# Kernel optimization log

Measured on AMD Instinct MI355X. Metric: run time of the kernel, lower is better.

Reference implementation:

```python
import jax, jax.numpy as jnp
import numpy as np

B, N, H = 128, 256, 1024


def setup_inputs() -> dict:
    key = jax.random.key(0)
    ks = jax.random.split(key, 10)
    s = 1.0 / np.sqrt(H)
    return {
        "encoder_outputs": jax.random.normal(ks[0], (B, N, H), jnp.float32),
        "W_ih": jax.random.normal(ks[1], (4 * H, H), jnp.float32) * s,
        "W_hh": jax.random.normal(ks[2], (4 * H, H), jnp.float32) * s,
        "b_ih": jax.random.normal(ks[3], (4 * H,), jnp.float32) * s,
        "b_hh": jax.random.normal(ks[4], (4 * H,), jnp.float32) * s,
        "Wa": jax.random.normal(ks[5], (H, H), jnp.float32) * s,
        "Ua": jax.random.normal(ks[6], (H, H), jnp.float32) * s,
        "v": jax.random.normal(ks[7], (H,), jnp.float32) * s,
        "start_token": jax.random.uniform(ks[8], (H,), jnp.float32, -0.1, 0.1),
        "end_token": jax.random.uniform(ks[9], (H,), jnp.float32, -0.1, 0.1),
    }


def reference(encoder_outputs, W_ih, W_hh, b_ih, b_hh, Wa, Ua, v, start_token, end_token):
    b, n, h = encoder_outputs.shape
    # extended encoder outputs: [B, N+1, H] (end token appended)
    ext = jnp.concatenate([encoder_outputs, jnp.broadcast_to(end_token, (b, 1, h))], axis=1)
    enc_Wa = ext @ Wa.T  # loop-invariant W_a projection, [B, N+1, H]

    def step(carry, _):
        hx, cx, mask, x = carry
        # LSTMCell
        gates = x @ W_ih.T + b_ih + hx @ W_hh.T + b_hh  # [B, 4H]
        i_g, f_g, g_g, o_g = jnp.split(gates, 4, axis=1)
        cx = jax.nn.sigmoid(f_g) * cx + jax.nn.sigmoid(i_g) * jnp.tanh(g_g)
        hx = jax.nn.sigmoid(o_g) * jnp.tanh(cx)
        # additive attention scores over N+1 slots
        scores = jnp.einsum('bnh,h->bn', jnp.tanh(enc_Wa + (hx @ Ua.T)[:, None, :]), v)
        scores = jnp.where(mask, -jnp.inf, scores)
        log_probs = jax.nn.log_softmax(scores, axis=1)
        next_idx = jnp.argmax(log_probs, axis=1)  # greedy (no teacher forcing)
        # mask selected input nodes only (end token at index N stays selectable)
        upd = (jnp.arange(n + 1)[None, :] == next_idx[:, None]) & (next_idx < n)[:, None]
        mask = mask | upd
        # per-batch gather: decoder_input = ext[b, next_idx[b]] (row N == end_token)
        x = jnp.take_along_axis(ext, next_idx[:, None, None], axis=1)[:, 0, :]
        return (hx, cx, mask, x), (log_probs, next_idx)

    init = (
        jnp.zeros((b, h), jnp.float32),
        jnp.zeros((b, h), jnp.float32),
        jnp.zeros((b, n + 1), bool),
        jnp.broadcast_to(start_token, (b, h)),
    )
    _, (log_probs, idxs) = jax.lax.scan(step, init, None, length=n + 1)
    # [T, B, ...] -> [B, T, ...]
    return jnp.swapaxes(log_probs, 0, 1), jnp.swapaxes(idxs, 0, 1)
```

## Files before the change

kernel.cpp:

```cpp
#include <hip/hip_runtime.h>
#include <math.h>

#define BB 128
#define NN 256
#define NP1 257
#define HH 1024

typedef unsigned char u8;
typedef unsigned short u16;
typedef unsigned int u32;
typedef unsigned long long u64;
typedef __attribute__((ext_vector_type(8))) short short8v;
typedef __attribute__((ext_vector_type(4))) short short4v;
typedef __attribute__((ext_vector_type(4))) float float4v;

__device__ __forceinline__ u16 f2b(float x) {
    union { float f; u32 u; } c; c.f = x;
    u32 r = (c.u + 0x7fffu + ((c.u >> 16) & 1u)) >> 16;
    return (u16)r;
}
__device__ __forceinline__ float b2f(u16 s) {
    union { u32 u; float f; } c; c.u = ((u32)s) << 16;
    return c.f;
}
__device__ __forceinline__ float ftanh(float x) {
    float e = __builtin_amdgcn_exp2f(x * 2.8853900817779268f);
    return 1.f - 2.f * __builtin_amdgcn_rcpf(e + 1.f);
}
__device__ __forceinline__ float fsig(float x) {
    return __builtin_amdgcn_rcpf(1.f + __builtin_amdgcn_exp2f(x * -1.4426950408889634f));
}

__device__ __forceinline__ u8 f2e8(float x) {
    u32 u = __float_as_uint(x);
    u32 sgn = (u >> 24) & 0x80u;
    float ax = __uint_as_float(u & 0x7fffffffu);
    if (!(ax < 448.f)) return (u8)(sgn | 0x7Eu);
    if (ax < 0.015625f) {
        int q = (int)rintf(ax * 512.f);
        if (q >= 8) return (u8)(sgn | 0x08u);
        return (u8)(sgn | (u32)q);
    }
    u32 au = u & 0x7fffffffu;
    au += 0x7ffffu + ((au >> 20) & 1u);
    int e = (int)(au >> 23) - 127;
    u32 m3 = (au >> 20) & 7u;
    if (e > 8 || (e == 8 && m3 == 7)) return (u8)(sgn | 0x7Eu);
    return (u8)(sgn | ((u32)(e + 7) << 3) | m3);
}
__device__ __forceinline__ float e82f(u32 u) {
    u32 t = ((u & 0x80u) << 24) | ((u & 0x7Fu) << 20);
    return __uint_as_float(t) * 0x1p+120f;
}

__device__ __forceinline__ u64 gload64(const u16* p) {
    return __hip_atomic_load((u64*)p, __ATOMIC_RELAXED, __HIP_MEMORY_SCOPE_AGENT);
}
__device__ __forceinline__ u64 gload64b(const u8* p) {
    return __hip_atomic_load((const u64*)p, __ATOMIC_RELAXED, __HIP_MEMORY_SCOPE_AGENT);
}
__device__ __forceinline__ short8v gload8h(const u16* p) {
    union { u64 q[2]; short8v v; } uq;
    uq.q[0] = gload64(p);
    uq.q[1] = gload64(p + 4);
    return uq.v;
}
__device__ __forceinline__ void gstore32(u32* p, u32 v) {
    __hip_atomic_store(p, v, __ATOMIC_RELAXED, __HIP_MEMORY_SCOPE_AGENT);
}
__device__ __forceinline__ u32 gload32(const u32* p) {
    return __hip_atomic_load((u32*)p, __ATOMIC_RELAXED, __HIP_MEMORY_SCOPE_AGENT);
}

#define CPHI(m) ((m) + (((m) >> 5) << 2))
#define SWZ(r, c) (((r) << 6) + ((((c) ^ ((r) & 7))) << 3))
#define HPHI(c) ((c) + ((c) >> 5))

#define GBAR() do {                                        \
    asm volatile("s_waitcnt lgkmcnt(0)" ::: "memory");     \
    __builtin_amdgcn_s_barrier();                          \
} while (0)

__device__ __forceinline__ void pbar(int* slots, int* go, int gen) {
    asm volatile("" ::: "memory");
    __syncthreads();
    const int t = threadIdx.x;
    if (blockIdx.x == 0) {
        if (t >= 1 && t < 256) {
            while ((int)gload32((u32*)&slots[t << 4]) < gen)
                __builtin_amdgcn_s_sleep(1);
        }
        __syncthreads();
        if (t == 0) gstore32((u32*)go, (u32)gen);
    } else {
        if (t == 0) {
            gstore32((u32*)&slots[blockIdx.x << 4], (u32)gen);
            while ((int)gload32((u32*)go) < gen)
                __builtin_amdgcn_s_sleep(1);
        }
        __syncthreads();
    }
    asm volatile("" ::: "memory");
}

__global__ __launch_bounds__(256) void k_binit(float* cx, u16* hxbA, int* mask,
                                               int* cur, int* slots, int* go,
                                               int* cflag, int* nlist, int* cnt) {
    int i = blockIdx.x * 256 + threadIdx.x;
    if (i < BB * HH) cx[i] = 0.f;
    if (i < BB * HH / 2) ((u32*)hxbA)[i] = 0u;
    if (i < BB * NP1) { mask[i] = 0; nlist[i] = i % NP1; }
    if (i < BB) { cur[i] = -1; cnt[i] = NP1; }
    if (i < 256 * 16) slots[i] = 0;
    if (i < BB * 16) cflag[i] = 0;
    if (i == 0) *go = 0;
}

__global__ __launch_bounds__(256) void k_pack(const float* __restrict__ Wih,
                                              const float* __restrict__ Whh,
                                              const float* __restrict__ bih,
                                              const float* __restrict__ bhh,
                                              u16* __restrict__ Wpk,
                                              float* __restrict__ bpk) {
    const int jp = blockIdx.x;
    const int nt = jp >> 6, r = jp & 63, g = r >> 4, c = r & 15;
    const int j = g * HH + nt * 16 + c;
    const int t = threadIdx.x;
    const int k = t * 8;
    const float* s = (k < HH) ? (Wih + (size_t)j * HH + k)
                              : (Whh + (size_t)j * HH + (k - HH));
    float4 v0 = *(const float4*)(s);
    float4 v1 = *(const float4*)(s + 4);
    short8v o;
    o[0]=(short)f2b(v0.x); o[1]=(short)f2b(v0.y); o[2]=(short)f2b(v0.z); o[3]=(short)f2b(v0.w);
    o[4]=(short)f2b(v1.x); o[5]=(short)f2b(v1.y); o[6]=(short)f2b(v1.z); o[7]=(short)f2b(v1.w);
    *(short8v*)(Wpk + (size_t)jp * 2048 + k) = o;
    if (t == 0) bpk[jp] = bih[j] + bhh[j];
}

__global__ __launch_bounds__(256) void k_cvte(const float* __restrict__ enc,
                                              const float* __restrict__ etok,
                                              const float* __restrict__ stok,
                                              u16* __restrict__ encB) {
    const int row = blockIdx.x;
    const float* src = (row < BB * NN) ? enc + (size_t)row * HH
                      : (row == BB * NN ? etok : stok);
    const int t = threadIdx.x;
    float4 v = *(const float4*)(src + t * 4);
    short4v o;
    o[0]=(short)f2b(v.x); o[1]=(short)f2b(v.y); o[2]=(short)f2b(v.z); o[3]=(short)f2b(v.w);
    *(short4v*)(encB + (size_t)row * HH + t * 4) = o;
}

__global__ __launch_bounds__(256) void k_cvtu(const float* __restrict__ Ua,
                                              u16* __restrict__ Uab) {
    const int row = blockIdx.x;
    const int t = threadIdx.x;
    float4 v = *(const float4*)(Ua + (size_t)row * HH + t * 4);
    short4v o;
    o[0]=(short)f2b(v.x); o[1]=(short)f2b(v.y); o[2]=(short)f2b(v.z); o[3]=(short)f2b(v.w);
    *(short4v*)(Uab + (size_t)row * HH + t * 4) = o;
}

__global__ __launch_bounds__(256, 2) void k_encWa8(const float* __restrict__ enc,
                                                   const float* __restrict__ etok,
                                                   const float* __restrict__ Wa,
                                                   u8* __restrict__ out) {
    __shared__ float As[32][140];
    __shared__ float Ws[32][140];
    const int mt = blockIdx.x, ntl = blockIdx.y;
    const int tid = threadIdx.x;
    const int lr = tid >> 2, lc = tid & 3;
    const int tr = tid & 15, tc = tid >> 4;

    const int r0 = mt * 128 + lr, r1 = r0 + 64;
    const int bb0 = r0 / NP1, nn0 = r0 - bb0 * NP1;
    const int bb1 = r1 / NP1, nn1 = r1 - bb1 * NP1;
    const float* a0 = (nn0 == NN) ? etok : enc + ((size_t)(bb0 * NN + nn0)) * HH;
    const float* a1 = (nn1 == NN) ? etok : enc + ((size_t)(bb1 * NN + nn1)) * HH;
    const float* w0 = Wa + (size_t)(ntl * 128 + lr) * HH;
    const float* w1 = w0 + (size_t)64 * HH;
    const int ca = CPHI(lr), cb = CPHI(lr + 64);
    const int colA = tr * 8 + ((tr >> 2) << 2);
    const int colB = tc * 8 + ((tc >> 2) << 2);

    float acc[8][8] = {};
    for (int k0 = 0; k0 < HH; k0 += 32) {
        float4 va0 = *(const float4*)(a0 + k0 + lc * 4);
        float4 va1 = *(const float4*)(a0 + k0 + lc * 4 + 16);
        float4 va2 = *(const float4*)(a1 + k0 + lc * 4);
        float4 va3 = *(const float4*)(a1 + k0 + lc * 4 + 16);
        float4 vb0 = *(const float4*)(w0 + k0 + lc * 4);
        float4 vb1 = *(const float4*)(w0 + k0 + lc * 4 + 16);
        float4 vb2 = *(const float4*)(w1 + k0 + lc * 4);
        float4 vb3 = *(const float4*)(w1 + k0 + lc * 4 + 16);
        __syncthreads();
        #pragma unroll
        for (int e = 0; e < 4; e++) {
            As[lc*4+e][ca]      = ((const float*)&va0)[e];
            As[lc*4+16+e][ca]   = ((const float*)&va1)[e];
            As[lc*4+e][cb]      = ((const float*)&va2)[e];
            As[lc*4+16+e][cb]   = ((const float*)&va3)[e];
            Ws[lc*4+e][ca]      = ((const float*)&vb0)[e];
            Ws[lc*4+16+e][ca]   = ((const float*)&vb1)[e];
            Ws[lc*4+e][cb]      = ((const float*)&vb2)[e];
            Ws[lc*4+16+e][cb]   = ((const float*)&vb3)[e];
        }
        __syncthreads();
        #pragma unroll
        for (int kk = 0; kk < 32; kk++) {
            float4 A0 = *(const float4*)&As[kk][colA];
            float4 A1 = *(const float4*)&As[kk][colA + 4];
            float4 B0 = *(const float4*)&Ws[kk][colB];
            float4 B1 = *(const float4*)&Ws[kk][colB + 4];
            float av[8] = {A0.x,A0.y,A0.z,A0.w,A1.x,A1.y,A1.z,A1.w};
            float bv[8] = {B0.x,B0.y,B0.z,B0.w,B1.x,B1.y,B1.z,B1.w};
            #pragma unroll
            for (int i = 0; i < 8; i++)
                #pragma unroll
                for (int j = 0; j < 8; j++) acc[i][j] += av[i] * bv[j];
        }
        __syncthreads();
    }
    #pragma unroll
    for (int i = 0; i < 8; i++) {
        u64 pk = 0;
        #pragma unroll
        for (int j = 0; j < 8; j++)
            pk |= (u64)f2e8(acc[i][j]) << (8 * j);
        *(u64*)(out + (size_t)(mt * 128 + tr * 8 + i) * HH + ntl * 128 + tc * 8) = pk;
    }
}

__global__ __launch_bounds__(512, 1) void k_persist(
    const u16* __restrict__ encB, const u16* __restrict__ Wpk,
    const float* __restrict__ bpk, const u16* __restrict__ Uab,
    const u8* __restrict__ encWa8, const float* __restrict__ vvec,
    int* __restrict__ cur, int* __restrict__ mask,
    u16* __restrict__ hxbA, u16* __restrict__ hxbB,
    float* __restrict__ cx, float* __restrict__ hup,
    float* __restrict__ scSg, int* __restrict__ cflag,
    int* __restrict__ nlist, int* __restrict__ cnt,
    float* __restrict__ out_lp, float* __restrict__ out_idx,
    int* __restrict__ slots, int* __restrict__ go)
{
    __shared__ u16 AsX[32 * 64];
    __shared__ u16 BsX[64 * 64];
    __shared__ u16 AsH[32 * 64];
    __shared__ u16 BsH[64 * 64];
    __shared__ float Gs[8][32][17];
    __shared__ float huS[HH + 32];
    __shared__ float vvS[HH + 32];
    __shared__ float rv[32];
    __shared__ int   ri[16];
    __shared__ int   nlS[NP1];
    __shared__ int   posS;

    const int bid = blockIdx.x;
    const int t = threadIdx.x;
    const int wv = t >> 6, lane = t & 63;
    const int tg = t & 255, w4 = (t >> 6) & 3;
    int gen = 1;

    for (int step = 0; step < NP1; step++) {
        const u16* hin = (step & 1) ? hxbB : hxbA;
        u16* hout = (step & 1) ? hxbA : hxbB;

        {
            const int nt = bid & 63, mt = bid >> 6;
            const int rA = tg >> 3, koA = (tg & 7) * 8;
            const int cA16 = tg & 7;
            const int rB = tg >> 2, koB = (tg & 3) * 16;
            const int cB16 = (tg & 3) * 2;
            const int mg = mt * 32 + rA;

            short8v apre[16];
            short8v b0_pf[3], b1_pf[3];
            const u16* brow = nullptr;
            if (t < 256) {
                const int sel = (int)gload32((const u32*)&cur[mg]);
                const u16* xrow = encB + (size_t)((sel < 0) ? (BB * NN + 1)
                             : (sel == NN ? BB * NN : (mg * NN + sel))) * HH;
                #pragma unroll
                for (int i = 0; i < 16; i++)
                    apre[i] = *(const short8v*)(xrow + i * 64 + koA);
                brow = Wpk + (size_t)(nt * 64 + rB) * 2048;
            } else {
                const u16* hrow = hin + (size_t)mg * HH;
                #pragma unroll
                for (int i = 0; i < 16; i++)
                    apre[i] = gload8h(hrow + i * 64 + koA);
                brow = Wpk + (size_t)(nt * 64 + rB) * 2048 + HH;
            }
            #pragma unroll
            for (int d = 0; d < 3; d++) {
                b0_pf[d] = *(const short8v*)(brow + d * 64 + koB);
                b1_pf[d] = *(const short8v*)(brow + d * 64 + koB + 8);
            }
            float4v acc0 = {}, acc1 = {};
            #pragma unroll
            for (int it = 0; it < 16; ++it) {
                GBAR();
                if (t < 256) {
                    *(short8v*)&AsX[SWZ(rA, cA16)] = apre[it];
                    *(short8v*)&BsX[SWZ(rB, cB16)] = b0_pf[it % 3];
                    *(short8v*)&BsX[SWZ(rB, cB16 + 1)] = b1_pf[it % 3];
                } else {
                    *(short8v*)&AsH[SWZ(rA, cA16)] = apre[it];
                    *(short8v*)&BsH[SWZ(rB, cB16)] = b0_pf[it % 3];
                    *(short8v*)&BsH[SWZ(rB, cB16 + 1)] = b1_pf[it % 3];
                }
                GBAR();
                if (it + 3 < 16) {
                    b0_pf[it % 3] = *(const short8v*)(brow + (it + 3) * 64 + koB);
                    b1_pf[it % 3] = *(const short8v*)(brow + (it + 3) * 64 + koB + 8);
                }
                if (t < 256) {
                    #pragma unroll
                    for (int kf = 0; kf < 2; ++kf) {
                        const int c16 = kf * 4 + (lane >> 4);
                        short8v bf = *(const short8v*)&BsX[SWZ(w4 * 16 + (lane & 15), c16)];
                        short8v a0 = *(const short8v*)&AsX[SWZ(lane & 15, c16)];
                        short8v a1 = *(const short8v*)&AsX[SWZ(16 + (lane & 15), c16)];
                        acc0 = __builtin_amdgcn_mfma_f32_16x16x32_bf16(a0, bf, acc0, 0, 0, 0);
                        acc1 = __builtin_amdgcn_mfma_f32_16x16x32_bf16(a1, bf, acc1, 0, 0, 0);
                    }
                } else {
                    #pragma unroll
                    for (int kf = 0; kf < 2; ++kf) {
                        const int c16 = kf * 4 + (lane >> 4);
                        short8v bf = *(const short8v*)&BsH[SWZ(w4 * 16 + (lane & 15), c16)];
                        short8v a0 = *(const short8v*)&AsH[SWZ(lane & 15, c16)];
                        short8v a1 = *(const short8v*)&AsH[SWZ(16 + (lane & 15), c16)];
                        acc0 = __builtin_amdgcn_mfma_f32_16x16x32_bf16(a0, bf, acc0, 0, 0, 0);
                        acc1 = __builtin_amdgcn_mfma_f32_16x16x32_bf16(a1, bf, acc1, 0, 0, 0);
                    }
                }
            }
            __syncthreads();
            #pragma unroll
            for (int r = 0; r < 4; r++) {
                Gs[wv][(lane >> 4) * 4 + r][lane & 15]      = acc0[r];
                Gs[wv][16 + (lane >> 4) * 4 + r][lane & 15] = acc1[r];
            }
            __syncthreads();
            if (t < 256) {
                const int m = t >> 3, cpr = (t & 7) * 2;
                const int mg2 = mt * 32 + m;
                float hn2[2];
                #pragma unroll
                for (int e = 0; e < 2; e++) {
                    const int c = cpr + e;
                    float gi  = Gs[0][m][c] + Gs[4][m][c] + bpk[nt * 64 + c];
                    float gf  = Gs[1][m][c] + Gs[5][m][c] + bpk[nt * 64 + 16 + c];
                    float gg  = Gs[2][m][c] + Gs[6][m][c] + bpk[nt * 64 + 32 + c];
                    float go2 = Gs[3][m][c] + Gs[7][m][c] + bpk[nt * 64 + 48 + c];
                    const int cg = nt * 16 + c;
                    float cold = cx[(size_t)mg2 * HH + cg];
                    float cn = fsig(gf) * cold + fsig(gi) * ftanh(gg);
                    hn2[e] = fsig(go2) * ftanh(cn);
                    cx[(size_t)mg2 * HH + cg] = cn;
                }
                u32 pk = (u32)f2b(hn2[0]) | ((u32)f2b(hn2[1]) << 16);
                gstore32((u32*)(hout + (size_t)mg2 * HH + nt * 16 + cpr), pk);
            }
        }
        pbar(slots, go, gen++);

        {
            const int nt2 = bid & 15, mt2 = (bid >> 4) & 3, ks = bid >> 6;
            const int rA = tg >> 3, koA = (tg & 7) * 8;
            const int cA16 = tg & 7;
            const int rB = tg >> 2, koB = (tg & 3) * 16;
            const int cB16 = (tg & 3) * 2;
            short8v hb[4];
            short8v ub0[2], ub1[2];
            const u16* brow = nullptr;
            if (t < 256) {
                const u16* arow = hout + (size_t)(mt2 * 32 + rA) * HH + ks * 256;
                #pragma unroll
                for (int i = 0; i < 4; i++)
                    hb[i] = gload8h(arow + i * 64 + koA);
                brow = Uab + (size_t)(nt2 * 64 + rB) * HH + ks * 256;
                #pragma unroll
                for (int d = 0; d < 2; d++) {
                    ub0[d] = *(const short8v*)(brow + d * 64 + koB);
                    ub1[d] = *(const short8v*)(brow + d * 64 + koB + 8);
                }
            }
            float4v acc0 = {}, acc1 = {};
            #pragma unroll
            for (int it = 0; it < 4; ++it) {
                GBAR();
                if (t < 256) {
                    *(short8v*)&AsX[SWZ(rA, cA16)] = hb[it];
                    *(short8v*)&BsX[SWZ(rB, cB16)] = ub0[it & 1];
                    *(short8v*)&BsX[SWZ(rB, cB16 + 1)] = ub1[it & 1];
                }
                GBAR();
                if (t < 256) {
                    if (it + 2 < 4) {
                        ub0[it & 1] = *(const short8v*)(brow + (it + 2) * 64 + koB);
                        ub1[it & 1] = *(const short8v*)(brow + (it + 2) * 64 + koB + 8);
                    }
                    #pragma unroll
                    for (int kf = 0; kf < 2; ++kf) {
                        const int c16 = kf * 4 + (lane >> 4);
                        short8v bf = *(const short8v*)&BsX[SWZ(w4 * 16 + (lane & 15), c16)];
                        short8v a0 = *(const short8v*)&AsX[SWZ(lane & 15, c16)];
                        short8v a1 = *(const short8v*)&AsX[SWZ(16 + (lane & 15), c16)];
                        acc0 = __builtin_amdgcn_mfma_f32_16x16x32_bf16(a0, bf, acc0, 0, 0, 0);
                        acc1 = __builtin_amdgcn_mfma_f32_16x16x32_bf16(a1, bf, acc1, 0, 0, 0);
                    }
                }
            }
            if (t < 256) {
                const int n = nt2 * 64 + w4 * 16 + (lane & 15);
                #pragma unroll
                for (int r = 0; r < 4; r++) {
                    const int m0 = mt2 * 32 + (lane >> 4) * 4 + r;
                    gstore32((u32*)&hup[((size_t)ks * BB + m0) * HH + n],
                             __float_as_uint(acc0[r]));
                    gstore32((u32*)&hup[((size_t)ks * BB + m0 + 16) * HH + n],
                             __float_as_uint(acc1[r]));
                }
            }
        }
        pbar(slots, go, gen++);

        int cntb_v = 0;
        {
            const int qb = bid >> 7, b = bid & 127;
            #pragma unroll
            for (int cc = 0; cc < 2; cc++) {
                const int c = t + cc * 512;
                float s = 0.f;
                #pragma unroll
                for (int ks = 0; ks < 4; ks++)
                    s += __uint_as_float(gload32((const u32*)&hup[((size_t)ks * BB + b) * HH + c]));
                huS[HPHI(c)] = s;
                vvS[HPHI(c)] = vvec[c];
            }
            cntb_v = (int)gload32((const u32*)&cnt[b]);
            for (int i = t; i < cntb_v; i += 512)
                nlS[i] = (int)gload32((const u32*)&nlist[b * NP1 + i]);
            __syncthreads();

            const int half = (cntb_v + 1) >> 1;
            const int iend = qb ? cntb_v : half;
            const int istart = (qb ? half : 0) + wv * 4;
            const int c0 = lane * 16;

            auto loadrow = [&](int ii, u64& A, u64& B) {
                const int idx = nlS[(ii < iend) ? ii : (iend - 1)];
                const u8* rp = encWa8 + ((size_t)b * NP1 + idx) * HH + c0;
                A = gload64b(rp);
                B = gload64b(rp + 8);
            };
            auto rowscore = [&](u64 p0, u64 p1) -> float {
                float s = 0.f;
                #pragma unroll
                for (int j = 0; j < 8; j++)
                    s += vvS[HPHI(c0 + j)] * ftanh(e82f((u32)(p0 >> (8 * j)) & 0xFFu) + huS[HPHI(c0 + j)]);
                #pragma unroll
                for (int j = 0; j < 8; j++)
                    s += vvS[HPHI(c0 + 8 + j)] * ftanh(e82f((u32)(p1 >> (8 * j)) & 0xFFu) + huS[HPHI(c0 + 8 + j)]);
                #pragma unroll
                for (int off = 32; off; off >>= 1) s += __shfl_down(s, off);
                return s;
            };

            if (istart < iend) {
                u64 qa0, qc0, qa1, qc1, qa2, qc2, qa3, qc3;
                loadrow(istart + 0, qa0, qc0);
                loadrow(istart + 1, qa1, qc1);
                loadrow(istart + 2, qa2, qc2);
                loadrow(istart + 3, qa3, qc3);
                for (int i = istart; i < iend; i += 32) {
                    u64 pa0, pc0, pa1, pc1, pa2, pc2, pa3, pc3;
                    const int inext = i + 32;
                    if (inext < iend) {
                        loadrow(inext + 0, pa0, pc0);
                        loadrow(inext + 1, pa1, pc1);
                        loadrow(inext + 2, pa2, pc2);
                        loadrow(inext + 3, pa3, pc3);
                    } else {
                        pa0 = qa0; pc0 = qc0; pa1 = qa1; pc1 = qc1;
                        pa2 = qa2; pc2 = qc2; pa3 = qa3; pc3 = qc3;
                    }
                    float s0 = rowscore(qa0, qc0);
                    float s1 = rowscore(qa1, qc1);
                    float s2 = rowscore(qa2, qc2);
                    float s3 = rowscore(qa3, qc3);
                    if (lane == 0) {
                        gstore32((u32*)&scSg[b * NP1 + nlS[i]], __float_as_uint(s0));
                        if (i + 1 < iend)
                            gstore32((u32*)&scSg[b * NP1 + nlS[i + 1]], __float_as_uint(s1));
                        if (i + 2 < iend)
                            gstore32((u32*)&scSg[b * NP1 + nlS[i + 2]], __float_as_uint(s2));
                        if (i + 3 < iend)
                            gstore32((u32*)&scSg[b * NP1 + nlS[i + 3]], __float_as_uint(s3));
                    }
                    qa0 = pa0; qc0 = pc0; qa1 = pa1; qc1 = pc1;
                    qa2 = pa2; qc2 = pc2; qa3 = pa3; qc3 = pc3;
                }
            }
            __syncthreads();
            if (qb == 1 && t == 0) gstore32((u32*)&cflag[b << 4], (u32)(step + 1));
        }

        if (bid < 128) {
            const int b = bid;
            if (t == 0) {
                while ((int)gload32((const u32*)&cflag[b << 4]) <= step)
                    __builtin_amdgcn_s_sleep(1);
            }
            __syncthreads();

            float va = -INFINITY;
            if (t < NP1) {
                float sc = __uint_as_float(gload32((const u32*)&scSg[b * NP1 + t]));
                va = (mask[b * NP1 + t] != 0) ? -INFINITY : sc;
            }
            float mv = va; int mi = t;
            #pragma unroll
            for (int off = 32; off; off >>= 1) {
                float ov = __shfl_down(mv, off);
                int   oi = __shfl_down(mi, off);
                if (ov > mv || (ov == mv && oi < mi)) { mv = ov; mi = oi; }
            }
            if (lane == 0) { rv[wv] = mv; ri[wv] = mi; }
            __syncthreads();
            if (t == 0) {
                float bv2 = rv[0]; int bi2 = ri[0];
                #pragma unroll
                for (int j2 = 1; j2 < 8; j2++)
                    if (rv[j2] > bv2 || (rv[j2] == bv2 && ri[j2] < bi2)) {
                        bv2 = rv[j2]; bi2 = ri[j2];
                    }
                rv[8] = bv2; ri[8] = bi2;
            }
            __syncthreads();
            const float vmax = rv[8]; const int amax = ri[8];

            float ss = (t < NP1) ? expf(va - vmax) : 0.f;
            #pragma unroll
            for (int off = 32; off; off >>= 1) ss += __shfl_down(ss, off);
            if (lane == 0) rv[16 + wv] = ss;
            __syncthreads();
            if (t == 0) {
                float s8 = 0.f;
                #pragma unroll
                for (int j2 = 0; j2 < 8; j2++) s8 += rv[16 + j2];
                rv[25] = s8;
            }
            __syncthreads();
            const float lse = vmax + logf(rv[25]);

            if (t < NP1)
                out_lp[((size_t)b * NP1 + step) * NP1 + t] = fmaxf(va - lse, -1e30f);

            if (t == 0) posS = -1;
            __syncthreads();
            if (t < cntb_v && nlS[t] == amax) posS = t;
            __syncthreads();
            if (t == 0) {
                if (amax < NN && posS >= 0) {
                    gstore32((u32*)&nlist[b * NP1 + posS], (u32)nlS[cntb_v - 1]);
                    gstore32((u32*)&cnt[b], (u32)(cntb_v - 1));
                }
                out_idx[(size_t)b * NP1 + step] = (float)amax;
                gstore32((u32*)&cur[b], (u32)amax);
                if (amax < NN) mask[b * NP1 + amax] = 1;
            }
        }
        pbar(slots, go, gen++);
    }
}

extern "C" void kernel_launch(void* const* d_in, const int* in_sizes, int n_in,
                              void* d_out, int out_size, void* d_ws, size_t ws_size,
                              hipStream_t stream) {
    const float* enc  = (const float*)d_in[0];
    const float* Wih  = (const float*)d_in[1];
    const float* Whh  = (const float*)d_in[2];
    const float* bih  = (const float*)d_in[3];
    const float* bhh  = (const float*)d_in[4];
    const float* Wa   = (const float*)d_in[5];
    const float* Ua   = (const float*)d_in[6];
    const float* v    = (const float*)d_in[7];
    const float* stok = (const float*)d_in[8];
    const float* etok = (const float*)d_in[9];
    float* out = (float*)d_out;
    float* out_idx = out + (size_t)BB * NP1 * NP1;

    size_t off = 0;
    char* base = (char*)d_ws;
    auto alloc = [&](size_t bytes) -> char* {
        char* p = base + off;
        off += (bytes + 255) & ~(size_t)255;
        return p;
    };
    u8*    encWa8 = (u8*)   alloc((size_t)BB * NP1 * HH);
    u16*   encB   = (u16*)  alloc((size_t)(BB * NN + 2) * HH * 2);
    u16*   Wpk    = (u16*)  alloc((size_t)4096 * 2048 * 2);
    u16*   Uab    = (u16*)  alloc((size_t)HH * HH * 2);
    float* bpk    = (float*)alloc((size_t)4096 * 4);
    float* hup    = (float*)alloc((size_t)4 * BB * HH * 4);
    float* cx     = (float*)alloc((size_t)BB * HH * 4);
    u16*   hxbA   = (u16*)  alloc((size_t)BB * HH * 2);
    u16*   hxbB   = (u16*)  alloc((size_t)BB * HH * 2);
    float* scSg   = (float*)alloc((size_t)BB * NP1 * 4);
    int*   mask   = (int*)  alloc((size_t)BB * NP1 * 4);
    int*   nlist  = (int*)  alloc((size_t)BB * NP1 * 4);
    int*   cnt    = (int*)  alloc((size_t)BB * 4);
    int*   cur    = (int*)  alloc((size_t)BB * 4);
    int*   slots  = (int*)  alloc((size_t)256 * 16 * 4);
    int*   go     = (int*)  alloc((size_t)64);
    int*   cflag  = (int*)  alloc((size_t)BB * 16 * 4);
    if (off > ws_size) return;

    k_binit<<<512, 256, 0, stream>>>(cx, hxbA, mask, cur, slots, go, cflag,
                                     nlist, cnt);
    k_pack<<<4096, 256, 0, stream>>>(Wih, Whh, bih, bhh, Wpk, bpk);
    k_cvte<<<BB * NN + 2, 256, 0, stream>>>(enc, etok, stok, encB);
    k_cvtu<<<HH, 256, 0, stream>>>(Ua, Uab);
    k_encWa8<<<dim3(257, 8), 256, 0, stream>>>(enc, etok, Wa, encWa8);

    void* args[] = { (void*)&encB, (void*)&Wpk, (void*)&bpk, (void*)&Uab,
                     (void*)&encWa8, (void*)&v, (void*)&cur, (void*)&mask,
                     (void*)&hxbA, (void*)&hxbB, (void*)&cx, (void*)&hup,
                     (void*)&scSg, (void*)&cflag, (void*)&nlist, (void*)&cnt,
                     (void*)&out, (void*)&out_idx, (void*)&slots, (void*)&go };
    hipLaunchCooperativeKernel((const void*)k_persist, dim3(256), dim3(512),
                               args, 0, stream);
}
```

Baseline: 8.516 ms.

## Replace end-of-step grid barrier with per-row flags; load B fragments directly to registers

Drops the grid-wide barrier at the end of each decode step. Each batch row now publishes a per-row done flag after writing its chosen index, and the LSTM GEMM phase waits only on the 32 rows it needs. The MFMA weight (B) fragments for the LSTM and Ua GEMMs are now loaded straight from global into registers in MFMA layout, so they are no longer staged through shared memory. The A tiles are double-buffered in LDS, halving the block barriers per k-iteration. This cuts synchronization and LDS traffic per step, in exchange for uncoalesced B loads and more register pressure, plus a flag-based ordering that depends on correct memory fences.

Result: no change. 8.675 ms (+1.9%).

```diff
diff --git a/kernel.cpp b/kernel.cpp
--- a/kernel.cpp
+++ b/kernel.cpp
@@ -105,14 +105,15 @@
 
 __global__ __launch_bounds__(256) void k_binit(float* cx, u16* hxbA, int* mask,
                                                int* cur, int* slots, int* go,
-                                               int* cflag, int* nlist, int* cnt) {
+                                               int* cflag, int* nlist, int* cnt,
+                                               int* dflag) {
     int i = blockIdx.x * 256 + threadIdx.x;
     if (i < BB * HH) cx[i] = 0.f;
     if (i < BB * HH / 2) ((u32*)hxbA)[i] = 0u;
     if (i < BB * NP1) { mask[i] = 0; nlist[i] = i % NP1; }
     if (i < BB) { cur[i] = -1; cnt[i] = NP1; }
     if (i < 256 * 16) slots[i] = 0;
-    if (i < BB * 16) cflag[i] = 0;
+    if (i < BB * 16) { cflag[i] = 0; dflag[i] = 0; }
     if (i == 0) *go = 0;
 }
 
@@ -241,13 +242,14 @@
     float* __restrict__ cx, float* __restrict__ hup,
     float* __restrict__ scSg, int* __restrict__ cflag,
     int* __restrict__ nlist, int* __restrict__ cnt,
+    int* __restrict__ dflag,
     float* __restrict__ out_lp, float* __restrict__ out_idx,
     int* __restrict__ slots, int* __restrict__ go)
 {
-    __shared__ u16 AsX[32 * 64];
-    __shared__ u16 BsX[64 * 64];
-    __shared__ u16 AsH[32 * 64];
-    __shared__ u16 BsH[64 * 64];
+    __shared__ u16 AsX0[32 * 64];
+    __shared__ u16 AsX1[32 * 64];
+    __shared__ u16 AsH0[32 * 64];
+    __shared__ u16 AsH1[32 * 64];
     __shared__ float Gs[8][32][17];
     __shared__ float huS[HH + 32];
     __shared__ float vvS[HH + 32];
@@ -270,13 +272,17 @@
             const int nt = bid & 63, mt = bid >> 6;
             const int rA = tg >> 3, koA = (tg & 7) * 8;
             const int cA16 = tg & 7;
-            const int rB = tg >> 2, koB = (tg & 3) * 16;
-            const int cB16 = (tg & 3) * 2;
             const int mg = mt * 32 + rA;
+            u16* bufA0 = (t < 256) ? AsX0 : AsH0;
+            u16* bufA1 = (t < 256) ? AsX1 : AsH1;
+
+            if (t < 32) {
+                while ((int)gload32((const u32*)&dflag[(mt * 32 + t) << 4]) < step)
+                    __builtin_amdgcn_s_sleep(1);
+            }
+            __syncthreads();
 
             short8v apre[16];
-            short8v b0_pf[3], b1_pf[3];
-            const u16* brow = nullptr;
             if (t < 256) {
                 const int sel = (int)gload32((const u32*)&cur[mg]);
                 const u16* xrow = encB + (size_t)((sel < 0) ? (BB * NN + 1)
@@ -284,60 +290,45 @@
                 #pragma unroll
                 for (int i = 0; i < 16; i++)
                     apre[i] = *(const short8v*)(xrow + i * 64 + koA);
-                brow = Wpk + (size_t)(nt * 64 + rB) * 2048;
             } else {
                 const u16* hrow = hin + (size_t)mg * HH;
                 #pragma unroll
                 for (int i = 0; i < 16; i++)
                     apre[i] = gload8h(hrow + i * 64 + koA);
-                brow = Wpk + (size_t)(nt * 64 + rB) * 2048 + HH;
-            }
+            }
+            const u16* bfbase = Wpk
+                + (size_t)(nt * 64 + w4 * 16 + (lane & 15)) * 2048
+                + ((t < 256) ? 0 : HH) + ((lane >> 4) * 8);
+            short8v bfr[4][2];
             #pragma unroll
             for (int d = 0; d < 3; d++) {
-                b0_pf[d] = *(const short8v*)(brow + d * 64 + koB);
-                b1_pf[d] = *(const short8v*)(brow + d * 64 + koB + 8);
-            }
+                bfr[d][0] = *(const short8v*)(bfbase + d * 64);
+                bfr[d][1] = *(const short8v*)(bfbase + d * 64 + 32);
+            }
+
+            *(short8v*)&bufA0[SWZ(rA, cA16)] = apre[0];
+            GBAR();
             float4v acc0 = {}, acc1 = {};
             #pragma unroll
             for (int it = 0; it < 16; ++it) {
+                u16* rd = (it & 1) ? bufA1 : bufA0;
+                u16* wr = (it & 1) ? bufA0 : bufA1;
+                if (it < 15)
+                    *(short8v*)&wr[SWZ(rA, cA16)] = apre[it + 1];
+                if (it + 3 < 16) {
+                    bfr[(it + 3) & 3][0] = *(const short8v*)(bfbase + (it + 3) * 64);
+                    bfr[(it + 3) & 3][1] = *(const short8v*)(bfbase + (it + 3) * 64 + 32);
+                }
+                #pragma unroll
+                for (int kf = 0; kf < 2; ++kf) {
+                    const int c16 = kf * 4 + (lane >> 4);
+                    short8v a0 = *(const short8v*)&rd[SWZ(lane & 15, c16)];
+                    short8v a1 = *(const short8v*)&rd[SWZ(16 + (lane & 15), c16)];
+                    acc0 = __builtin_amdgcn_mfma_f32_16x16x32_bf16(a0, bfr[it & 3][kf], acc0, 0, 0, 0);
+                    acc1 = __builtin_amdgcn_mfma_f32_16x16x32_bf16(a1, bfr[it & 3][kf], acc1, 0, 0, 0);
+                }
                 GBAR();
-                if (t < 256) {
-                    *(short8v*)&AsX[SWZ(rA, cA16)] = apre[it];
-                    *(short8v*)&BsX[SWZ(rB, cB16)] = b0_pf[it % 3];
-                    *(short8v*)&BsX[SWZ(rB, cB16 + 1)] = b1_pf[it % 3];
-                } else {
-                    *(short8v*)&AsH[SWZ(rA, cA16)] = apre[it];
-                    *(short8v*)&BsH[SWZ(rB, cB16)] = b0_pf[it % 3];
-                    *(short8v*)&BsH[SWZ(rB, cB16 + 1)] = b1_pf[it % 3];
-                }
-                GBAR();
-                if (it + 3 < 16) {
-                    b0_pf[it % 3] = *(const short8v*)(brow + (it + 3) * 64 + koB);
-                    b1_pf[it % 3] = *(const short8v*)(brow + (it + 3) * 64 + koB + 8);
-                }
-                if (t < 256) {
-                    #pragma unroll
-                    for (int kf = 0; kf < 2; ++kf) {
-                        const int c16 = kf * 4 + (lane >> 4);
-                        short8v bf = *(const short8v*)&BsX[SWZ(w4 * 16 + (lane & 15), c16)];
-                        short8v a0 = *(const short8v*)&AsX[SWZ(lane & 15, c16)];
-                        short8v a1 = *(const short8v*)&AsX[SWZ(16 + (lane & 15), c16)];
-                        acc0 = __builtin_amdgcn_mfma_f32_16x16x32_bf16(a0, bf, acc0, 0, 0, 0);
-                        acc1 = __builtin_amdgcn_mfma_f32_16x16x32_bf16(a1, bf, acc1, 0, 0, 0);
-                    }
-                } else {
-                    #pragma unroll
-                    for (int kf = 0; kf < 2; ++kf) {
-                        const int c16 = kf * 4 + (lane >> 4);
-                        short8v bf = *(const short8v*)&BsH[SWZ(w4 * 16 + (lane & 15), c16)];
-                        short8v a0 = *(const short8v*)&AsH[SWZ(lane & 15, c16)];
-                        short8v a1 = *(const short8v*)&AsH[SWZ(16 + (lane & 15), c16)];
-                        acc0 = __builtin_amdgcn_mfma_f32_16x16x32_bf16(a0, bf, acc0, 0, 0, 0);
-                        acc1 = __builtin_amdgcn_mfma_f32_16x16x32_bf16(a1, bf, acc1, 0, 0, 0);
-                    }
-                }
-            }
-            __syncthreads();
+            }
             #pragma unroll
             for (int r = 0; r < 4; r++) {
                 Gs[wv][(lane >> 4) * 4 + r][lane & 15]      = acc0[r];
@@ -371,48 +362,42 @@
             const int nt2 = bid & 15, mt2 = (bid >> 4) & 3, ks = bid >> 6;
             const int rA = tg >> 3, koA = (tg & 7) * 8;
             const int cA16 = tg & 7;
-            const int rB = tg >> 2, koB = (tg & 3) * 16;
-            const int cB16 = (tg & 3) * 2;
             short8v hb[4];
-            short8v ub0[2], ub1[2];
-            const u16* brow = nullptr;
+            short8v ub[4][2];
             if (t < 256) {
                 const u16* arow = hout + (size_t)(mt2 * 32 + rA) * HH + ks * 256;
                 #pragma unroll
                 for (int i = 0; i < 4; i++)
                     hb[i] = gload8h(arow + i * 64 + koA);
-                brow = Uab + (size_t)(nt2 * 64 + rB) * HH + ks * 256;
-                #pragma unroll
-                for (int d = 0; d < 2; d++) {
-                    ub0[d] = *(const short8v*)(brow + d * 64 + koB);
-                    ub1[d] = *(const short8v*)(brow + d * 64 + koB + 8);
-                }
-            }
+                const u16* ubase = Uab
+                    + (size_t)(nt2 * 64 + w4 * 16 + (lane & 15)) * HH
+                    + ks * 256 + ((lane >> 4) * 8);
+                #pragma unroll
+                for (int d = 0; d < 4; d++) {
+                    ub[d][0] = *(const short8v*)(ubase + d * 64);
+                    ub[d][1] = *(const short8v*)(ubase + d * 64 + 32);
+                }
+            }
+            if (t < 256) *(short8v*)&AsX0[SWZ(rA, cA16)] = hb[0];
+            GBAR();
             float4v acc0 = {}, acc1 = {};
             #pragma unroll
             for (int it = 0; it < 4; ++it) {
-                GBAR();
+                u16* rd = (it & 1) ? AsX1 : AsX0;
+                u16* wr = (it & 1) ? AsX0 : AsX1;
                 if (t < 256) {
-                    *(short8v*)&AsX[SWZ(rA, cA16)] = hb[it];
-                    *(short8v*)&BsX[SWZ(rB, cB16)] = ub0[it & 1];
-                    *(short8v*)&BsX[SWZ(rB, cB16 + 1)] = ub1[it & 1];
-                }
-                GBAR();
-                if (t < 256) {
-                    if (it + 2 < 4) {
-                        ub0[it & 1] = *(const short8v*)(brow + (it + 2) * 64 + koB);
-                        ub1[it & 1] = *(const short8v*)(brow + (it + 2) * 64 + koB + 8);
-                    }
+                    if (it < 3)
+                        *(short8v*)&wr[SWZ(rA, cA16)] = hb[it + 1];
                     #pragma unroll
                     for (int kf = 0; kf < 2; ++kf) {
                         const int c16 = kf * 4 + (lane >> 4);
-                        short8v bf = *(const short8v*)&BsX[SWZ(w4 * 16 + (lane & 15), c16)];
-                        short8v a0 = *(const short8v*)&AsX[SWZ(lane & 15, c16)];
-                        short8v a1 = *(const short8v*)&AsX[SWZ(16 + (lane & 15), c16)];
-                        acc0 = __builtin_amdgcn_mfma_f32_16x16x32_bf16(a0, bf, acc0, 0, 0, 0);
-                        acc1 = __builtin_amdgcn_mfma_f32_16x16x32_bf16(a1, bf, acc1, 0, 0, 0);
+                        short8v a0 = *(const short8v*)&rd[SWZ(lane & 15, c16)];
+                        short8v a1 = *(const short8v*)&rd[SWZ(16 + (lane & 15), c16)];
+                        acc0 = __builtin_amdgcn_mfma_f32_16x16x32_bf16(a0, ub[it][kf], acc0, 0, 0, 0);
+                        acc1 = __builtin_amdgcn_mfma_f32_16x16x32_bf16(a1, ub[it][kf], acc1, 0, 0, 0);
                     }
                 }
+                GBAR();
             }
             if (t < 256) {
                 const int n = nt2 * 64 + w4 * 16 + (lane & 15);
@@ -572,9 +557,10 @@
                 out_idx[(size_t)b * NP1 + step] = (float)amax;
                 gstore32((u32*)&cur[b], (u32)amax);
                 if (amax < NN) mask[b * NP1 + amax] = 1;
-            }
-        }
-        pbar(slots, go, gen++);
+                asm volatile("s_waitcnt vmcnt(0)" ::: "memory");
+                gstore32((u32*)&dflag[b << 4], (u32)(step + 1));
+            }
+        }
     }
 }
 
@@ -618,10 +604,11 @@
     int*   slots  = (int*)  alloc((size_t)256 * 16 * 4);
     int*   go     = (int*)  alloc((size_t)64);
     int*   cflag  = (int*)  alloc((size_t)BB * 16 * 4);
+    int*   dflag  = (int*)  alloc((size_t)BB * 16 * 4);
     if (off > ws_size) return;
 
     k_binit<<<512, 256, 0, stream>>>(cx, hxbA, mask, cur, slots, go, cflag,
-                                     nlist, cnt);
+                                     nlist, cnt, dflag);
     k_pack<<<4096, 256, 0, stream>>>(Wih, Whh, bih, bhh, Wpk, bpk);
     k_cvte<<<BB * NN + 2, 256, 0, stream>>>(enc, etok, stok, encB);
     k_cvtu<<<HH, 256, 0, stream>>>(Ua, Uab);
@@ -631,6 +618,7 @@
                      (void*)&encWa8, (void*)&v, (void*)&cur, (void*)&mask,
                      (void*)&hxbA, (void*)&hxbB, (void*)&cx, (void*)&hup,
                      (void*)&scSg, (void*)&cflag, (void*)&nlist, (void*)&cnt,
+                     (void*)&dflag,
                      (void*)&out, (void*)&out_idx, (void*)&slots, (void*)&go };
     hipLaunchCooperativeKernel((const void*)k_persist, dim3(256), dim3(512),
                                args, 0, stream);
```
